# Optimization experiments

Hardware: AMD Instinct MI355X
Metric: run time of the kernel (lower is better)

The kernel has to match this reference:

```python
import jax, jax.numpy as jnp
import numpy as np
from jax.scipy.stats import norm as jnorm

B, S, D, H, E, K, FF = 8, 256, 1024, 16, 4, 2, 4096
HD = D // H
NOISE_EPS = 0.01
LOSS_COEF = 0.01
EPS_FILL = float(np.finfo(float).eps)


def _ln(x, g, b):
    m = x.mean(-1, keepdims=True)
    v = x.var(-1, keepdims=True)
    return (x - m) * jax.lax.rsqrt(v + 1e-5) * g + b


def setup_inputs() -> dict:
    key = jax.random.key(0)
    ks = jax.random.split(key, 16)
    r = lambda i, shape, s=1.0: jax.random.normal(ks[i], shape, dtype=jnp.float32) * s
    return {
        "x": r(0, (B, S, D)),
        "e_outputs": r(1, (B, 64, D)),            # unused (is_lm=True) but part of signature
        "noise": r(2, (B, E)),                     # the randn_like(clean_logits) draw
        "w_gate": r(3, (D, E), 0.02),
        "w_noise": r(4, (D, E), 0.02),
        "Wq": r(5, (E, D, D), 0.02),
        "Wk": r(6, (E, D, D), 0.02),
        "Wv": r(7, (E, D, D), 0.02),
        "Wo": r(8, (E, D, D), 0.02),
        "W1": r(9, (E, D, FF), 0.02),
        "b1": jnp.zeros((E, FF), jnp.float32),
        "W2": r(10, (E, FF, D), 0.02),
        "b2": jnp.zeros((E, D), jnp.float32),
        "g1": jnp.ones((E, D), jnp.float32),
        "be1": jnp.zeros((E, D), jnp.float32),
        "g2": jnp.ones((E, D), jnp.float32),
        "be2": jnp.zeros((E, D), jnp.float32),
        "trg_mask": jnp.tril(jnp.ones((S, S), dtype=bool))[None, None],  # causal [1,1,S,S]
        "src_mask": jnp.ones((1, 1, 1, 64), dtype=bool),                 # unused (is_lm=True)
    }


def _cv_squared(v):
    # torch .var() is unbiased (ddof=1)
    return v.var(ddof=1) / (v.mean() ** 2 + 1e-10)


def reference(x, e_outputs, noise, w_gate, w_noise, Wq, Wk, Wv, Wo, W1, b1, W2, b2,
              g1, be1, g2, be2, trg_mask, src_mask):
    b, s, d = x.shape
    # ---- noisy top-k gating (per sample, on the sequence-sum) ----
    xs = x.sum(axis=1)                                   # [B, D]
    clean = xs @ w_gate                                  # [B, E]
    raw_noise = xs @ w_noise                             # [B, E]
    stddev = jax.nn.softplus(raw_noise) + NOISE_EPS      # train=True -> *1.0
    noisy = clean + noise * stddev                       # logits
    top_logits, top_idx = jax.lax.top_k(noisy, K + 1)    # [B, K+1]
    topk_gates = jax.nn.softmax(top_logits[:, :K], axis=1)
    gates = jnp.zeros_like(noisy).at[jnp.arange(b)[:, None], top_idx[:, :K]].set(topk_gates)
    # load: prob each expert's clean logit lands in the noisy top-k
    thr_in = top_logits[:, K:K + 1]                      # (k+1)-th noisy value
    thr_out = top_logits[:, K - 1:K]                     # k-th noisy value
    is_in = noisy > thr_in
    prob = jnp.where(is_in,
                     jnorm.cdf((clean - thr_in) / stddev),
                     jnorm.cdf((clean - thr_out) / stddev))
    load = prob.sum(0)                                   # [E]
    importance = gates.sum(0)                            # [E]
    loss = (_cv_squared(importance) + _cv_squared(load)) * LOSS_COEF

    # ---- experts: standard decoder layer (self-attn + FFN), is_lm -> no cross-attn ----
    neg = jnp.asarray(-1e9, x.dtype)
    scale = 1.0 / np.sqrt(HD)

    def expert(p):
        wq, wk, wv, wo, w1, bb1, w2, bb2, gg1, bbe1, gg2, bbe2 = p
        q = (x @ wq).reshape(b, s, H, HD)
        k_ = (x @ wk).reshape(b, s, H, HD)
        v = (x @ wv).reshape(b, s, H, HD)
        scores = jnp.einsum('bqhd,bkhd->bhqk', q, k_) * scale
        scores = jnp.where(trg_mask, scores, neg)
        attn = jax.nn.softmax(scores, axis=-1)
        o = jnp.einsum('bhqk,bkhd->bqhd', attn, v).reshape(b, s, d) @ wo
        h = _ln(x + o, gg1, bbe1)
        ff = jax.nn.relu(h @ w1 + bb1) @ w2 + bb2
        return _ln(h + ff, gg2, bbe2)

    outs = jax.vmap(expert)((Wq, Wk, Wv, Wo, W1, b1, W2, b2, g1, be1, g2, be2))  # [E,B,S,D]

    # ---- combine: scatter-add of gate-weighted expert outputs (dense equivalent) ----
    y = jnp.einsum('be,ebsd->bsd', gates, outs)
    y = jnp.where(y == 0, jnp.asarray(EPS_FILL, y.dtype), y)
    return y, loss
```

## Files before the change

kernel.cpp:

```cpp
#include <hip/hip_runtime.h>
#include <hip/hip_bf16.h>

typedef __bf16 bf16;
typedef __attribute__((ext_vector_type(4))) __bf16 bf16x4;
typedef __attribute__((ext_vector_type(8))) __bf16 bf16x8;
typedef __attribute__((ext_vector_type(4))) float floatx4;

constexpr int CB = 8, CS = 256, CD = 1024, CH = 16, CE = 4, CFF = 4096, CHD = 64;
constexpr long long DD  = 1048576;
constexpr long long DFF = 4194304;
constexpr long long BSD = 2097152;
constexpr long long PSD = 4194304;

constexpr size_t OFF_PART = 0;
constexpr size_t OFF_CLEAN= 262144;
constexpr size_t OFF_RAW  = 262272;
constexpr size_t OFF_GATES= 262400;
constexpr size_t OFF_EACT = 262528;
constexpr size_t OFF_PBE  = 262592;
constexpr size_t OFF_BP   = 262656;
constexpr size_t OFF_XBF  = 263168;
constexpr size_t OFF_WT   = OFF_XBF + (size_t)BSD*2;
constexpr size_t OFF_W1T  = OFF_WT  + (size_t)16*DD*2;
constexpr size_t OFF_W2T  = OFF_W1T + (size_t)4*DFF*2;
constexpr size_t OFF_QKV  = OFF_W2T + (size_t)4*DFF*2;
constexpr size_t OFF_AO   = OFF_QKV + (size_t)3*PSD*2;
constexpr size_t OFF_F1   = OFF_QKV;
constexpr size_t OFF_PB   = OFF_AO  + (size_t)PSD*2;
constexpr size_t OFF_VT   = OFF_PB;
constexpr size_t OFF_H    = OFF_PB  + (size_t)2*PSD*4;
constexpr size_t OFF_HBF  = OFF_H   + (size_t)PSD*4;

__global__ __launch_bounds__(256)
void wtrans_cvt(const float* __restrict__ Wq, const float* __restrict__ Wk,
                const float* __restrict__ Wv, const float* __restrict__ Wo,
                const float* __restrict__ W1, const float* __restrict__ W2,
                bf16* __restrict__ wT, bf16* __restrict__ w1T, bf16* __restrict__ w2T,
                const float* __restrict__ x, bf16* __restrict__ xbf, float* __restrict__ part) {
  int zb = blockIdx.x;
  if (zb >= 3072) {
    int blk = zb - 3072;
    int b = blk >> 3, ch = blk & 7;
    int t = threadIdx.x;
    float s0 = 0.f, s1 = 0.f, s2 = 0.f, s3 = 0.f;
    long long base4 = ((long long)(b*CS + ch*32))*CD / 4;
#pragma unroll 4
    for (int r = 0; r < 32; ++r) {
      long long i4 = base4 + (long long)r*(CD/4) + t;
      float4 v = ((const float4*)x)[i4];
      bf16x4 o; o[0] = (bf16)v.x; o[1] = (bf16)v.y; o[2] = (bf16)v.z; o[3] = (bf16)v.w;
      ((bf16x4*)xbf)[i4] = o;
      s0 += v.x; s1 += v.y; s2 += v.z; s3 += v.w;
    }
    float4 sv; sv.x = s0; sv.y = s1; sv.z = s2; sv.w = s3;
    ((float4*)(part + (long long)blk*CD))[t] = sv;
    return;
  }
  int w = threadIdx.x >> 6;
  const float* src; bf16* d; int rows, cols, btk, btn;
  if (zb < 1024) {
    int m = zb >> 6, bt = zb & 63; int e = m >> 2; int which = m & 3;
    src = ((which == 0) ? Wq : (which == 1) ? Wk : (which == 2) ? Wv : Wo) + (long long)e*DD;
    d = wT + (long long)m*DD; rows = 1024; cols = 1024;
    btk = bt >> 3; btn = bt & 7;
  } else if (zb < 2048) {
    int z2 = zb - 1024; int e = z2 >> 8; int bt = z2 & 255;
    src = W1 + (long long)e*DFF; d = w1T + (long long)e*DFF;
    rows = 1024; cols = 4096; btk = bt >> 5; btn = bt & 31;
  } else {
    int z3 = zb - 2048; int e = z3 >> 8; int bt = z3 & 255;
    src = W2 + (long long)e*DFF; d = w2T + (long long)e*DFF;
    rows = 4096; cols = 1024; btk = bt >> 3; btn = bt & 7;
  }
  int tk = btk*2 + (w & 1);
  int tn = btn*2 + (w >> 1);
  int lane = threadIdx.x & 63;
  int ln = lane >> 3, lk = lane & 7;
  int k0 = tk*64, n0 = tn*64;
  const float* s = src + (long long)(k0 + lk*8)*cols + n0 + ln*8;
  floatx4 f[8][2];
#pragma unroll
  for (int j = 0; j < 8; ++j) {
    f[j][0] = __builtin_nontemporal_load((const floatx4*)(s + (long long)j*cols));
    f[j][1] = __builtin_nontemporal_load((const floatx4*)(s + (long long)j*cols + 4));
  }
  bf16* dp = d + (long long)(n0 + ln*8)*rows + k0 + lk*8;
#pragma unroll
  for (int jn = 0; jn < 8; ++jn) {
    bf16x8 o;
#pragma unroll
    for (int jk = 0; jk < 8; ++jk) {
      o[jk] = (bf16)f[jk][jn >> 2][jn & 3];
    }
    *(bf16x8*)(dp + (long long)jn*rows) = o;
  }
}

__global__ __launch_bounds__(256)
void gate_dots(const float* __restrict__ part, const float* __restrict__ wg,
               const float* __restrict__ wn, float* __restrict__ clean, float* __restrict__ raw) {
  int p = blockIdx.x, b = p >> 2, e = p & 3;
  int t = threadIdx.x;
  float s1 = 0.f, s2 = 0.f;
  for (int d = t; d < CD; d += 256) {
    float xv = 0.f;
#pragma unroll
    for (int c = 0; c < 8; ++c) xv += part[(long long)(b*8 + c)*CD + d];
    s1 += xv * wg[d*CE + e];
    s2 += xv * wn[d*CE + e];
  }
  for (int off = 32; off; off >>= 1) { s1 += __shfl_xor(s1, off); s2 += __shfl_xor(s2, off); }
  __shared__ float r1[4], r2[4];
  int lane = t & 63, w = t >> 6;
  if (lane == 0) { r1[w] = s1; r2[w] = s2; }
  __syncthreads();
  if (t == 0) { clean[p] = r1[0]+r1[1]+r1[2]+r1[3]; raw[p] = r2[0]+r2[1]+r2[2]+r2[3]; }
}

__global__ void gating_kernel(const float* __restrict__ clean, const float* __restrict__ raw,
                              const float* __restrict__ noise, float* __restrict__ gates,
                              int* __restrict__ eact, int* __restrict__ pairBE,
                              int* __restrict__ batchPair, float* __restrict__ loss_out) {
  if (threadIdx.x != 0) return;
  float imp[CE] = {0,0,0,0}, load[CE] = {0,0,0,0};
  int act[CE] = {0,0,0,0};
  for (int b = 0; b < CB; ++b) {
    float cl[CE], sd[CE], ny[CE];
    for (int e = 0; e < CE; ++e) {
      cl[e] = clean[b*CE + e];
      float rw = raw[b*CE + e];
      float sp = fmaxf(rw, 0.f) + log1pf(expf(-fabsf(rw)));
      sd[e] = sp + 0.01f;
      ny[e] = cl[e] + noise[b*CE + e]*sd[e];
    }
    int idx[CE] = {0,1,2,3};
    for (int a = 0; a < 3; ++a) {
      int best = a;
      for (int c = a + 1; c < 4; ++c) if (ny[idx[c]] > ny[idx[best]]) best = c;
      int tt = idx[a]; idx[a] = idx[best]; idx[best] = tt;
    }
    float l0 = ny[idx[0]], l1 = ny[idx[1]], l2 = ny[idx[2]];
    float e1 = expf(l1 - l0);
    float g0 = 1.f/(1.f + e1), g1v = e1/(1.f + e1);
    for (int e = 0; e < CE; ++e) gates[b*CE + e] = 0.f;
    gates[b*CE + idx[0]] = g0; gates[b*CE + idx[1]] = g1v;
    imp[idx[0]] += g0; imp[idx[1]] += g1v;
    act[idx[0]] = 1; act[idx[1]] = 1;
    for (int e = 0; e < CE; ++e) {
      bool is_in = ny[e] > l2;
      float thr = is_in ? l2 : l1;
      float zz = (cl[e] - thr) / sd[e];
      load[e] += 0.5f * erfcf(-zz * 0.70710678118654752440f);
    }
  }
  int pe2p[CB][CE];
  int pc = 0;
  for (int e = 0; e < CE; ++e)
    for (int b = 0; b < CB; ++b)
      if (gates[b*CE + e] != 0.f) { pairBE[pc] = b | (e << 8); pe2p[b][e] = pc; ++pc; }
  for (int b = 0; b < CB; ++b) {
    int s = 0;
    for (int e = 0; e < CE; ++e)
      if (gates[b*CE + e] != 0.f) batchPair[2*b + (s++)] = pe2p[b][e];
  }
  float m1 = 0.f, m2 = 0.f;
  for (int e = 0; e < CE; ++e) { m1 += imp[e]; m2 += load[e]; }
  m1 *= 0.25f; m2 *= 0.25f;
  float v1 = 0.f, v2 = 0.f;
  for (int e = 0; e < CE; ++e) { float d1 = imp[e]-m1, d2 = load[e]-m2; v1 += d1*d1; v2 += d2*d2; }
  v1 *= (1.f/3.f); v2 *= (1.f/3.f);
  loss_out[0] = 0.01f * (v1/(m1*m1 + 1e-10f) + v2/(m2*m2 + 1e-10f));
  for (int e = 0; e < CE; ++e) eact[e] = act[e];
}

__global__ __launch_bounds__(256)
void transpose_v(const bf16* __restrict__ qkvC, bf16* __restrict__ vTb) {
  int z = blockIdx.x; int p = z >> 4, h = z & 15;
  int w = threadIdx.x >> 6, lane = threadIdx.x & 63;
  int ln = lane >> 3, lk = lane & 7;
  const bf16* v = qkvC + 2*PSD + ((long long)(p*CS + w*64 + ln*8))*CD + h*CHD + lk*8;
  bf16x8 in[8];
#pragma unroll
  for (int j = 0; j < 8; ++j) in[j] = *(const bf16x8*)(v + (long long)j*CD);
  bf16* vt = vTb + ((long long)(p*CH + h)*CHD + lk*8)*CS + w*64 + ln*8;
#pragma unroll
  for (int dn = 0; dn < 8; ++dn) {
    bf16x8 o;
#pragma unroll
    for (int j = 0; j < 8; ++j) o[j] = in[j][dn];
    *(bf16x8*)(vt + (long long)dn*CS) = o;
  }
}

__device__ __forceinline__ void cp16(const bf16* g, bf16* l) {
  __builtin_amdgcn_global_load_lds((const __attribute__((address_space(1))) void*)g,
                                   (__attribute__((address_space(3))) void*)l, 16, 0, 0);
}

template<int R, int W>
__device__ __forceinline__ void stage(const bf16* __restrict__ src, int ld, bf16* dst) {
  constexpr int W8 = W/8;
  int t = threadIdx.x;
  int l = t & 63, wid = t >> 6;
#pragma unroll
  for (int i = 0; i < (R*W8)/256; ++i) {
    int idb = i*256 + wid*64;
    int id = idb + l;
    int row = id / W8, sl = id % W8;
    int gc = sl ^ (row & 7);
    cp16(src + (long long)row*ld + gc*8, dst + (long long)idb*8);
  }
}

__global__ __launch_bounds__(256)
void attn_fused(const bf16* __restrict__ qkvC, const bf16* __restrict__ vTb,
                bf16* __restrict__ aoC) {
  int h = blockIdx.x, p = blockIdx.y, qt = blockIdx.z;
  const bf16* qp = qkvC + (long long)(p*CS)*CD + h*CHD;
  const bf16* kp = qp + PSD;
  const bf16* vt = vTb + (long long)(p*CH + h)*CHD*CS;
  bf16* aop = aoC + (long long)(p*CS)*CD + h*CHD;

  __shared__ bf16 Ps[64*264];
  __shared__ float smaxL[64*4], ssumL[64*4], Lrow[64];

  int t = threadIdx.x, w = t >> 6, lane = t & 63, lr = lane & 15, quad = lane >> 4;

  floatx4 accs[4][4] = {};
  if (w <= qt) {
#pragma unroll
    for (int kk = 0; kk < 2; ++kk) {
      int c = kk*4 + quad;
      bf16x8 af[4], bfr[4];
#pragma unroll
      for (int i = 0; i < 4; ++i) {
        af[i]  = *(const bf16x8*)(qp + (long long)(qt*64 + i*16 + lr)*CD + c*8);
        bfr[i] = *(const bf16x8*)(kp + (long long)(w*64  + i*16 + lr)*CD + c*8);
      }
#pragma unroll
      for (int i = 0; i < 4; ++i)
#pragma unroll
        for (int j = 0; j < 4; ++j)
          accs[i][j] = __builtin_amdgcn_mfma_f32_16x16x32_bf16(af[i], bfr[j], accs[i][j], 0, 0, 0);
    }
  }
  float rmax[4][4];
#pragma unroll
  for (int i = 0; i < 4; ++i)
#pragma unroll
    for (int r = 0; r < 4; ++r) {
      int qrow = qt*64 + i*16 + quad*4 + r;
      float m = -3.0e38f;
#pragma unroll
      for (int j = 0; j < 4; ++j) {
        int kcol = w*64 + j*16 + lr;
        float s = accs[i][j][r]*0.125f;
        s = (kcol <= qrow) ? s : -3.0e38f;
        accs[i][j][r] = s;
        m = fmaxf(m, s);
      }
      rmax[i][r] = m;
    }
#pragma unroll
  for (int off = 1; off <= 8; off <<= 1)
#pragma unroll
    for (int i = 0; i < 4; ++i)
#pragma unroll
      for (int r = 0; r < 4; ++r) rmax[i][r] = fmaxf(rmax[i][r], __shfl_xor(rmax[i][r], off));
  if (lr == 0)
#pragma unroll
    for (int i = 0; i < 4; ++i)
#pragma unroll
      for (int r = 0; r < 4; ++r) smaxL[(i*16 + quad*4 + r)*4 + w] = rmax[i][r];
  __syncthreads();
  float rsum[4][4];
#pragma unroll
  for (int i = 0; i < 4; ++i)
#pragma unroll
    for (int r = 0; r < 4; ++r) {
      floatx4 mv = *(const floatx4*)&smaxL[(i*16 + quad*4 + r)*4];
      float M = fmaxf(fmaxf(mv[0], mv[1]), fmaxf(mv[2], mv[3]));
      float srow = 0.f;
#pragma unroll
      for (int j = 0; j < 4; ++j) {
        float pp = __expf(accs[i][j][r] - M);
        accs[i][j][r] = pp;
        srow += pp;
      }
      rsum[i][r] = srow;
    }
#pragma unroll
  for (int off = 1; off <= 8; off <<= 1)
#pragma unroll
    for (int i = 0; i < 4; ++i)
#pragma unroll
      for (int r = 0; r < 4; ++r) rsum[i][r] += __shfl_xor(rsum[i][r], off);
  if (lr == 0)
#pragma unroll
    for (int i = 0; i < 4; ++i)
#pragma unroll
      for (int r = 0; r < 4; ++r) ssumL[(i*16 + quad*4 + r)*4 + w] = rsum[i][r];
  __syncthreads();
  if (w == 0 && lr == 0) {
#pragma unroll
    for (int i = 0; i < 4; ++i)
#pragma unroll
      for (int r = 0; r < 4; ++r) {
        int m = i*16 + quad*4 + r;
        floatx4 sv = *(const floatx4*)&ssumL[m*4];
        Lrow[m] = sv[0] + sv[1] + sv[2] + sv[3];
      }
  }
  if (w <= qt) {
#pragma unroll
    for (int i = 0; i < 4; ++i)
#pragma unroll
      for (int j = 0; j < 4; ++j)
#pragma unroll
        for (int r = 0; r < 4; ++r)
          Ps[(i*16 + quad*4 + r)*264 + w*64 + j*16 + lr] = (bf16)accs[i][j][r];
  }
  __syncthreads();
  floatx4 acco[4] = {};
  int ksMax = (qt + 1)*2;
  for (int ks = 0; ks < ksMax; ++ks) {
    int c = ks*4 + quad;
    bf16x8 ap = *(const bf16x8*)(Ps + (w*16 + lr)*264 + c*8);
#pragma unroll
    for (int j = 0; j < 4; ++j) {
      bf16x8 bv = *(const bf16x8*)(vt + (long long)(j*16 + lr)*CS + c*8);
      acco[j] = __builtin_amdgcn_mfma_f32_16x16x32_bf16(ap, bv, acco[j], 0, 0, 0);
    }
  }
#pragma unroll
  for (int r = 0; r < 4; ++r) {
    int orow = w*16 + quad*4 + r;
    float inv = 1.f / Lrow[orow];
#pragma unroll
    for (int j = 0; j < 4; ++j)
      aop[(long long)(qt*64 + orow)*CD + j*16 + lr] = (bf16)(acco[j][r]*inv);
  }
}

__global__ __launch_bounds__(256)
void ln1_kernel(const float* __restrict__ x, const float* __restrict__ PbF,
                const float* __restrict__ gamma, const float* __restrict__ beta,
                float* __restrict__ h, bf16* __restrict__ hbf, const int* __restrict__ pairBE) {
  int row = blockIdx.x;
  int pbe = pairBE[row >> 8]; int pb = pbe & 255, pe = pbe >> 8;
  int t = threadIdx.x;
  float4 a = ((const float4*)(x + ((long long)pb*CS + (row & 255))*CD))[t];
  float4 b = ((const float4*)(PbF + (long long)row*CD))[t];
  float4 c = ((const float4*)(PbF + PSD + (long long)row*CD))[t];
  float v0 = a.x + b.x + c.x, v1 = a.y + b.y + c.y;
  float v2 = a.z + b.z + c.z, v3 = a.w + b.w + c.w;
  float s  = v0 + v1 + v2 + v3;
  float s2 = v0*v0 + v1*v1 + v2*v2 + v3*v3;
  int lane = t & 63, wave = t >> 6;
  for (int off = 32; off; off >>= 1) { s += __shfl_xor(s, off); s2 += __shfl_xor(s2, off); }
  __shared__ float red[8];
  if (lane == 0) { red[wave*2] = s; red[wave*2 + 1] = s2; }
  __syncthreads();
  s  = red[0] + red[2] + red[4] + red[6];
  s2 = red[1] + red[3] + red[5] + red[7];
  float mean = s * (1.f/CD);
  float rstd = rsqrtf(s2*(1.f/CD) - mean*mean + 1e-5f);
  float4 gm = ((const float4*)(gamma + (long long)pe*CD))[t];
  float4 bt = ((const float4*)(beta  + (long long)pe*CD))[t];
  float4 o;
  o.x = (v0 - mean)*rstd*gm.x + bt.x;
  o.y = (v1 - mean)*rstd*gm.y + bt.y;
  o.z = (v2 - mean)*rstd*gm.z + bt.z;
  o.w = (v3 - mean)*rstd*gm.w + bt.w;
  ((float4*)(h + (long long)row*CD))[t] = o;
  bf16x4 ob; ob[0] = (bf16)o.x; ob[1] = (bf16)o.y; ob[2] = (bf16)o.z; ob[3] = (bf16)o.w;
  ((bf16x4*)(hbf + (long long)row*CD))[t] = ob;
}

__global__ __launch_bounds__(256)
void ln2y_kernel(const float* __restrict__ h, const bf16* __restrict__ PbB,
                 const float* __restrict__ gamma, const float* __restrict__ beta,
                 float* __restrict__ y, const float* __restrict__ gates,
                 const int* __restrict__ pairBE, const int* __restrict__ batchPair) {
  int row = blockIdx.x;
  int b = row >> 8, sIdx = row & 255;
  int p0 = batchPair[2*b], p1 = batchPair[2*b + 1];
  int e0 = pairBE[p0] >> 8, e1 = pairBE[p1] >> 8;
  float gv0 = gates[b*CE + e0], gv1 = gates[b*CE + e1];
  long long r0 = (long long)p0*CS + sIdx, r1 = (long long)p1*CS + sIdx;
  int t = threadIdx.x;
  float4 a = ((const float4*)(h + r0*CD))[t];
  float4 c = ((const float4*)(h + r1*CD))[t];
#pragma unroll
  for (int k = 0; k < 4; ++k) {
    bf16x4 pa = ((const bf16x4*)(PbB + (long long)k*PSD + r0*CD))[t];
    bf16x4 pc = ((const bf16x4*)(PbB + (long long)k*PSD + r1*CD))[t];
    a.x += (float)pa[0]; a.y += (float)pa[1]; a.z += (float)pa[2]; a.w += (float)pa[3];
    c.x += (float)pc[0]; c.y += (float)pc[1]; c.z += (float)pc[2]; c.w += (float)pc[3];
  }
  float sA = a.x + a.y + a.z + a.w;
  float sA2 = a.x*a.x + a.y*a.y + a.z*a.z + a.w*a.w;
  float sB = c.x + c.y + c.z + c.w;
  float sB2 = c.x*c.x + c.y*c.y + c.z*c.z + c.w*c.w;
  int lane = t & 63, wave = t >> 6;
  for (int off = 32; off; off >>= 1) {
    sA += __shfl_xor(sA, off); sA2 += __shfl_xor(sA2, off);
    sB += __shfl_xor(sB, off); sB2 += __shfl_xor(sB2, off);
  }
  __shared__ float red[16];
  if (lane == 0) { red[wave*4] = sA; red[wave*4+1] = sA2; red[wave*4+2] = sB; red[wave*4+3] = sB2; }
  __syncthreads();
  sA  = red[0] + red[4] + red[8]  + red[12];
  sA2 = red[1] + red[5] + red[9]  + red[13];
  sB  = red[2] + red[6] + red[10] + red[14];
  sB2 = red[3] + red[7] + red[11] + red[15];
  float mA = sA*(1.f/CD), mB = sB*(1.f/CD);
  float rsA = rsqrtf(sA2*(1.f/CD) - mA*mA + 1e-5f);
  float rsB = rsqrtf(sB2*(1.f/CD) - mB*mB + 1e-5f);
  float4 gm0 = ((const float4*)(gamma + (long long)e0*CD))[t];
  float4 bt0 = ((const float4*)(beta  + (long long)e0*CD))[t];
  float4 gm1 = ((const float4*)(gamma + (long long)e1*CD))[t];
  float4 bt1 = ((const float4*)(beta  + (long long)e1*CD))[t];
  float4 o;
  o.x = gv0*((a.x - mA)*rsA*gm0.x + bt0.x) + gv1*((c.x - mB)*rsB*gm1.x + bt1.x);
  o.y = gv0*((a.y - mA)*rsA*gm0.y + bt0.y) + gv1*((c.y - mB)*rsB*gm1.y + bt1.y);
  o.z = gv0*((a.z - mA)*rsA*gm0.z + bt0.z) + gv1*((c.z - mB)*rsB*gm1.z + bt1.z);
  o.w = gv0*((a.w - mA)*rsA*gm0.w + bt0.w) + gv1*((c.w - mB)*rsB*gm1.w + bt1.w);
  constexpr float EF = 2.2204460492503131e-16f;
  o.x = (o.x == 0.f) ? EF : o.x;  o.y = (o.y == 0.f) ? EF : o.y;
  o.z = (o.z == 0.f) ? EF : o.z;  o.w = (o.w == 0.f) ? EF : o.w;
  ((float4*)(y + (long long)row*CD))[t] = o;
}

enum { EPI_BF16 = 0, EPI_F32 = 1, EPI_BRELU = 2, EPI_BIASBF16 = 3 };

template<int EPI, int KS, bool A_BATCH>
__global__ __launch_bounds__(256)
void gemm_nt(const bf16* __restrict__ A, const bf16* __restrict__ Bt, void* __restrict__ Cv,
             int K , int lda, int ldb, int ldc,
             long long oBe, long long oBmat, long long oCmat, long long oCk,
             const float* __restrict__ bias, long long biasStride,
             const int* __restrict__ pairBE) {
  constexpr int BM = 128, BN = 128;
  int z = blockIdx.z;
  int zk = z % KS, mat = z / KS;
  int gx = gridDim.x;
  int nwg = gx * gridDim.y;
  int lin = blockIdx.x + gx*blockIdx.y;
  int nl  = (lin & 7)*(nwg >> 3) + (lin >> 3);
  int m0 = (nl % gx) * BM, n0 = (nl / gx) * BN;
  int pbe = pairBE[m0 >> 8]; int pb = pbe & 255, pe = pbe >> 8;
  const bf16* Ab = A + (A_BATCH ? ((long long)pb*CS + (m0 & 255))*lda : (long long)m0*lda)
                     + (long long)zk*K;
  const bf16* Bb = Bt + (long long)pe*oBe + (long long)mat*oBmat + (long long)zk*K
                      + (long long)n0*ldb;
  long long coff = (long long)mat*oCmat + (long long)zk*oCk;

  __shared__ bf16 As[BM*64];
  __shared__ bf16 Bs[BN*64];

  int wave = threadIdx.x >> 6;
  int lane = threadIdx.x & 63;
  int wm = wave >> 1, wn = wave & 1;
  int lr = lane & 15;
  int quad = lane >> 4;

  floatx4 acc[4][4] = {};

  for (int kt = 0; kt < K; kt += 64) {
    stage<BM, 64>(Ab + kt, lda, As);
    stage<BN, 64>(Bb + kt, ldb, Bs);
    __syncthreads();
#pragma unroll
    for (int kk = 0; kk < 2; ++kk) {
      bf16x8 af[4], bfr[4];
#pragma unroll
      for (int i = 0; i < 4; ++i) {
        int c = kk*4 + quad;
        int m = wm*64 + i*16 + lr;
        af[i]  = *(const bf16x8*)(As + m*64 + ((c ^ (m & 7))*8));
        int n = wn*64 + i*16 + lr;
        bfr[i] = *(const bf16x8*)(Bs + n*64 + ((c ^ (n & 7))*8));
      }
#pragma unroll
      for (int i = 0; i < 4; ++i)
#pragma unroll
        for (int j = 0; j < 4; ++j)
          acc[i][j] = __builtin_amdgcn_mfma_f32_16x16x32_bf16(af[i], bfr[j], acc[i][j], 0, 0, 0);
    }
    __syncthreads();
  }

#pragma unroll
  for (int j = 0; j < 4; ++j) {
    int col = n0 + wn*64 + j*16 + lr;
    float bv = 0.f;
    if constexpr (EPI == EPI_BRELU || EPI == EPI_BIASBF16)
      if (zk == 0) bv = bias[(long long)pe*biasStride + col];
#pragma unroll
    for (int i = 0; i < 4; ++i) {
#pragma unroll
      for (int r = 0; r < 4; ++r) {
        int row = m0 + wm*64 + i*16 + quad*4 + r;
        float v = acc[i][j][r] + bv;
        long long idx = coff + (long long)row*ldc + col;
        if constexpr (EPI == EPI_BF16)          ((bf16*)Cv)[idx] = (bf16)v;
        else if constexpr (EPI == EPI_F32)      ((float*)Cv)[idx] = v;
        else if constexpr (EPI == EPI_BRELU)    ((bf16*)Cv)[idx] = (bf16)fmaxf(v, 0.f);
        else                                    ((bf16*)Cv)[idx] = (bf16)v;
      }
    }
  }
}

extern "C" void kernel_launch(void* const* d_in, const int* in_sizes, int n_in,
                              void* d_out, int out_size, void* d_ws, size_t ws_size,
                              hipStream_t stream) {
  const float* x       = (const float*)d_in[0];
  const float* noise   = (const float*)d_in[2];
  const float* w_gate  = (const float*)d_in[3];
  const float* w_noise = (const float*)d_in[4];
  const float* Wq      = (const float*)d_in[5];
  const float* Wk      = (const float*)d_in[6];
  const float* Wv      = (const float*)d_in[7];
  const float* Wo      = (const float*)d_in[8];
  const float* W1      = (const float*)d_in[9];
  const float* b1      = (const float*)d_in[10];
  const float* W2      = (const float*)d_in[11];
  const float* b2      = (const float*)d_in[12];
  const float* g1      = (const float*)d_in[13];
  const float* be1     = (const float*)d_in[14];
  const float* g2      = (const float*)d_in[15];
  const float* be2     = (const float*)d_in[16];

  char* ws = (char*)d_ws;
  float* y    = (float*)d_out;
  float* loss = y + (size_t)BSD;

  float* part  = (float*)(ws + OFF_PART);
  float* clean = (float*)(ws + OFF_CLEAN);
  float* raw   = (float*)(ws + OFF_RAW);
  float* gates = (float*)(ws + OFF_GATES);
  int*   eact  = (int*)  (ws + OFF_EACT);
  int*   pairBE= (int*)  (ws + OFF_PBE);
  int*   batchPair = (int*)(ws + OFF_BP);
  bf16*  xbf   = (bf16*) (ws + OFF_XBF);
  bf16*  wT    = (bf16*) (ws + OFF_WT);
  bf16*  w1T   = (bf16*) (ws + OFF_W1T);
  bf16*  w2T   = (bf16*) (ws + OFF_W2T);
  bf16*  qkvC  = (bf16*) (ws + OFF_QKV);
  bf16*  aoC   = (bf16*) (ws + OFF_AO);
  bf16*  f1    = (bf16*) (ws + OFF_F1);
  bf16*  vTb   = (bf16*) (ws + OFF_VT);
  float* PbF   = (float*)(ws + OFF_PB);
  bf16*  PbB   = (bf16*) (ws + OFF_PB);
  float* h     = (float*)(ws + OFF_H);
  bf16*  hbf   = (bf16*) (ws + OFF_HBF);

  wtrans_cvt<<<3136, 256, 0, stream>>>(Wq, Wk, Wv, Wo, W1, W2, wT, w1T, w2T, x, xbf, part);
  gate_dots<<<32, 256, 0, stream>>>(part, w_gate, w_noise, clean, raw);
  gating_kernel<<<1, 64, 0, stream>>>(clean, raw, noise, gates, eact, pairBE, batchPair, loss);

  gemm_nt<EPI_BF16, 1, true><<<dim3(32, 8, 3), 256, 0, stream>>>(
      xbf, wT, qkvC, 1024, 1024, 1024, 1024,
      4*DD, DD, PSD, 0, nullptr, 0, pairBE);

  transpose_v<<<256, 256, 0, stream>>>(qkvC, vTb);

  attn_fused<<<dim3(CH, 16, 4), 256, 0, stream>>>(qkvC, vTb, aoC);

  gemm_nt<EPI_F32, 2, false><<<dim3(32, 8, 2), 256, 0, stream>>>(
      aoC, wT + 3*DD, PbF, 512, 1024, 1024, 1024,
      4*DD, 0, 0, PSD, nullptr, 0, pairBE);

  ln1_kernel<<<4096, 256, 0, stream>>>(x, PbF, g1, be1, h, hbf, pairBE);

  gemm_nt<EPI_BRELU, 1, false><<<dim3(32, 32, 1), 256, 0, stream>>>(
      hbf, w1T, f1, 1024, 1024, 1024, 4096,
      DFF, 0, 0, 0, b1, CFF, pairBE);

  gemm_nt<EPI_BIASBF16, 4, false><<<dim3(32, 8, 4), 256, 0, stream>>>(
      f1, w2T, PbB, 1024, 4096, 4096, 1024,
      DFF, 0, 0, PSD, b2, CD, pairBE);

  ln2y_kernel<<<2048, 256, 0, stream>>>(h, PbB, g2, be2, y, gates, pairBE, batchPair);
}
```

Measured before the change: 489.8 us.

## Use 256x256 GEMM tiles with 512 threads and double-buffered async LDS staging

The shared NT GEMM kernel moves from 128x128 tiles on 4 waves to 256x256 tiles on 8 waves, with each wave computing 128x64. The A and B LDS tiles become double-buffered: the next k-slice is fetched with global_load_lds while the current one feeds the MFMAs, and syncthreads is replaced by explicit vmcnt waits plus raw barriers. The aim is more data reuse per load and hiding global-load latency. In exchange, each launch now has far fewer workgroups (128–256 blocks on a 256-CU part), LDS use roughly doubles to about 128KB, and the larger accumulator raises register pressure.

```diff
diff --git a/kernel.cpp b/kernel.cpp
--- a/kernel.cpp
+++ b/kernel.cpp
@@ -197,14 +197,14 @@
                                    (__attribute__((address_space(3))) void*)l, 16, 0, 0);
 }
 
-template<int R, int W>
-__device__ __forceinline__ void stage(const bf16* __restrict__ src, int ld, bf16* dst) {
+template<int R, int W, int NT>
+__device__ __forceinline__ void stageN(const bf16* __restrict__ src, int ld, bf16* dst) {
   constexpr int W8 = W/8;
   int t = threadIdx.x;
   int l = t & 63, wid = t >> 6;
 #pragma unroll
-  for (int i = 0; i < (R*W8)/256; ++i) {
-    int idb = i*256 + wid*64;
+  for (int i = 0; i < (R*W8)/NT; ++i) {
+    int idb = i*NT + wid*64;
     int id = idb + l;
     int row = id / W8, sl = id % W8;
     int gc = sl ^ (row & 7);
@@ -435,13 +435,13 @@
 enum { EPI_BF16 = 0, EPI_F32 = 1, EPI_BRELU = 2, EPI_BIASBF16 = 3 };
 
 template<int EPI, int KS, bool A_BATCH>
-__global__ __launch_bounds__(256)
+__global__ __launch_bounds__(512, 2)
 void gemm_nt(const bf16* __restrict__ A, const bf16* __restrict__ Bt, void* __restrict__ Cv,
              int K , int lda, int ldb, int ldc,
              long long oBe, long long oBmat, long long oCmat, long long oCk,
              const float* __restrict__ bias, long long biasStride,
              const int* __restrict__ pairBE) {
-  constexpr int BM = 128, BN = 128;
+  constexpr int BM = 256, BN = 256;
   int z = blockIdx.z;
   int zk = z % KS, mat = z / KS;
   int gx = gridDim.x;
@@ -456,39 +456,53 @@
                       + (long long)n0*ldb;
   long long coff = (long long)mat*oCmat + (long long)zk*oCk;
 
-  __shared__ bf16 As[BM*64];
-  __shared__ bf16 Bs[BN*64];
+  __shared__ bf16 As[2][BM*64];
+  __shared__ bf16 Bs[2][BN*64];
 
   int wave = threadIdx.x >> 6;
   int lane = threadIdx.x & 63;
-  int wm = wave >> 1, wn = wave & 1;
+  int wm = wave >> 2, wn = wave & 3;
   int lr = lane & 15;
   int quad = lane >> 4;
 
-  floatx4 acc[4][4] = {};
-
-  for (int kt = 0; kt < K; kt += 64) {
-    stage<BM, 64>(Ab + kt, lda, As);
-    stage<BN, 64>(Bb + kt, ldb, Bs);
-    __syncthreads();
+  floatx4 acc[8][4] = {};
+
+  int nt = K / 64;
+  stageN<BM, 64, 512>(Ab, lda, As[0]);
+  stageN<BN, 64, 512>(Bb, ldb, Bs[0]);
+  for (int t = 0; t < nt; ++t) {
+    int cur = t & 1;
+    if (t + 1 < nt) {
+      stageN<BM, 64, 512>(Ab + (t+1)*64, lda, As[cur ^ 1]);
+      stageN<BN, 64, 512>(Bb + (t+1)*64, ldb, Bs[cur ^ 1]);
+      asm volatile("s_waitcnt vmcnt(8)" ::: "memory");
+    } else {
+      asm volatile("s_waitcnt vmcnt(0)" ::: "memory");
+    }
+    __builtin_amdgcn_s_barrier();
+    asm volatile("" ::: "memory");
 #pragma unroll
     for (int kk = 0; kk < 2; ++kk) {
-      bf16x8 af[4], bfr[4];
-#pragma unroll
-      for (int i = 0; i < 4; ++i) {
-        int c = kk*4 + quad;
-        int m = wm*64 + i*16 + lr;
-        af[i]  = *(const bf16x8*)(As + m*64 + ((c ^ (m & 7))*8));
-        int n = wn*64 + i*16 + lr;
-        bfr[i] = *(const bf16x8*)(Bs + n*64 + ((c ^ (n & 7))*8));
+      int c = kk*4 + quad;
+      bf16x8 af[8], bfr[4];
+#pragma unroll
+      for (int i = 0; i < 8; ++i) {
+        int m = wm*128 + i*16 + lr;
+        af[i] = *(const bf16x8*)(As[cur] + m*64 + ((c ^ (m & 7))*8));
       }
 #pragma unroll
-      for (int i = 0; i < 4; ++i)
+      for (int j = 0; j < 4; ++j) {
+        int n = wn*64 + j*16 + lr;
+        bfr[j] = *(const bf16x8*)(Bs[cur] + n*64 + ((c ^ (n & 7))*8));
+      }
+#pragma unroll
+      for (int i = 0; i < 8; ++i)
 #pragma unroll
         for (int j = 0; j < 4; ++j)
           acc[i][j] = __builtin_amdgcn_mfma_f32_16x16x32_bf16(af[i], bfr[j], acc[i][j], 0, 0, 0);
     }
-    __syncthreads();
+    __builtin_amdgcn_s_barrier();
+    asm volatile("" ::: "memory");
   }
 
 #pragma unroll
@@ -498,10 +512,10 @@
     if constexpr (EPI == EPI_BRELU || EPI == EPI_BIASBF16)
       if (zk == 0) bv = bias[(long long)pe*biasStride + col];
 #pragma unroll
-    for (int i = 0; i < 4; ++i) {
+    for (int i = 0; i < 8; ++i) {
 #pragma unroll
       for (int r = 0; r < 4; ++r) {
-        int row = m0 + wm*64 + i*16 + quad*4 + r;
+        int row = m0 + wm*128 + i*16 + quad*4 + r;
         float v = acc[i][j][r] + bv;
         long long idx = coff + (long long)row*ldc + col;
         if constexpr (EPI == EPI_BF16)          ((bf16*)Cv)[idx] = (bf16)v;
@@ -561,7 +575,7 @@
   gate_dots<<<32, 256, 0, stream>>>(part, w_gate, w_noise, clean, raw);
   gating_kernel<<<1, 64, 0, stream>>>(clean, raw, noise, gates, eact, pairBE, batchPair, loss);
 
-  gemm_nt<EPI_BF16, 1, true><<<dim3(32, 8, 3), 256, 0, stream>>>(
+  gemm_nt<EPI_BF16, 1, true><<<dim3(16, 4, 3), 512, 0, stream>>>(
       xbf, wT, qkvC, 1024, 1024, 1024, 1024,
       4*DD, DD, PSD, 0, nullptr, 0, pairBE);
 
@@ -569,17 +583,17 @@
 
   attn_fused<<<dim3(CH, 16, 4), 256, 0, stream>>>(qkvC, vTb, aoC);
 
-  gemm_nt<EPI_F32, 2, false><<<dim3(32, 8, 2), 256, 0, stream>>>(
+  gemm_nt<EPI_F32, 2, false><<<dim3(16, 4, 2), 512, 0, stream>>>(
       aoC, wT + 3*DD, PbF, 512, 1024, 1024, 1024,
       4*DD, 0, 0, PSD, nullptr, 0, pairBE);
 
   ln1_kernel<<<4096, 256, 0, stream>>>(x, PbF, g1, be1, h, hbf, pairBE);
 
-  gemm_nt<EPI_BRELU, 1, false><<<dim3(32, 32, 1), 256, 0, stream>>>(
+  gemm_nt<EPI_BRELU, 1, false><<<dim3(16, 16, 1), 512, 0, stream>>>(
       hbf, w1T, f1, 1024, 1024, 1024, 4096,
       DFF, 0, 0, 0, b1, CFF, pairBE);
 
-  gemm_nt<EPI_BIASBF16, 4, false><<<dim3(32, 8, 4), 256, 0, stream>>>(
+  gemm_nt<EPI_BIASBF16, 4, false><<<dim3(16, 4, 4), 512, 0, stream>>>(
       f1, w2T, PbB, 1024, 4096, 4096, 1024,
       DFF, 0, 0, PSD, b2, CD, pairBE);
 
```

Result: no change. 488.9 us (-0.2%).
